# Kernel tuning notes

Measured on AMD Instinct MI355X. Metric: run time of the kernel, lower is better.

Reference implementation:

```python
import jax, jax.numpy as jnp
import numpy as np

# ODEBlock integrates dy/dt = f(t, y) from T0 to T1 with the dopri5 (Dormand-Prince RK45)
# stage structure. torchdiffeq's dopri5 is adaptive; for a jit/vjp-friendly reference we
# run the same 6-stage dopri5 tableau with a fixed number of steps (same per-step math).
T0, T1 = 0.0, 1.0
NUM_STEPS = 16

BATCH, D, H = 512, 1024, 2048


def setup_inputs() -> dict:
    key = jax.random.key(0)
    k0, k1, k2 = jax.random.split(key, 3)
    x = jax.random.normal(k0, (BATCH, D), dtype=jnp.float32)
    W1 = jax.random.normal(k1, (D, H), dtype=jnp.float32) / np.float32(np.sqrt(D))
    b1 = jnp.zeros((H,), dtype=jnp.float32)
    W2 = jax.random.normal(k2, (H, D), dtype=jnp.float32) / np.float32(np.sqrt(H))
    b2 = jnp.zeros((D,), dtype=jnp.float32)
    return {"x": x, "W1": W1, "b1": b1, "W2": W2, "b2": b2}


def reference(x, W1, b1, W2, b2):
    def f(t, y):
        # odefunc: 2-layer tanh MLP, autonomous in t
        return jnp.tanh(y @ W1 + b1) @ W2 + b2

    h = jnp.float32((T1 - T0) / NUM_STEPS)

    def step(carry, _):
        y, t = carry
        k1 = f(t, y)
        k2 = f(t + h * (1.0 / 5.0), y + h * (1.0 / 5.0) * k1)
        k3 = f(t + h * (3.0 / 10.0), y + h * ((3.0 / 40.0) * k1 + (9.0 / 40.0) * k2))
        k4 = f(t + h * (4.0 / 5.0),
               y + h * ((44.0 / 45.0) * k1 - (56.0 / 15.0) * k2 + (32.0 / 9.0) * k3))
        k5 = f(t + h * (8.0 / 9.0),
               y + h * ((19372.0 / 6561.0) * k1 - (25360.0 / 2187.0) * k2
                        + (64448.0 / 6561.0) * k3 - (212.0 / 729.0) * k4))
        k6 = f(t + h,
               y + h * ((9017.0 / 3168.0) * k1 - (355.0 / 33.0) * k2
                        + (46732.0 / 5247.0) * k3 + (49.0 / 176.0) * k4
                        - (5103.0 / 18656.0) * k5))
        # 5th-order solution weights (b7 = 0, so k7/FSAL not needed for the update)
        y_next = y + h * ((35.0 / 384.0) * k1 + (500.0 / 1113.0) * k3
                          + (125.0 / 192.0) * k4 - (2187.0 / 6784.0) * k5
                          + (11.0 / 84.0) * k6)
        return (y_next, t + h), None

    (y_final, _), _ = jax.lax.scan(step, (x, jnp.float32(T0)), None, length=NUM_STEPS)
    return y_final
```

## Files before the change

### kernel.cpp

```cpp
#include <hip/hip_runtime.h>
#include <hip/hip_bf16.h>

using bf16 = __hip_bfloat16;
typedef __attribute__((ext_vector_type(8))) short short8;
typedef __attribute__((ext_vector_type(4))) float f32x4;
typedef __attribute__((ext_vector_type(4))) unsigned short u16x4;

#define MFMA16(A, B, C) __builtin_amdgcn_mfma_f32_16x16x32_bf16(A, B, C, 0, 0, 0)

constexpr int Mdim = 512;
constexpr int Ddim = 1024;
constexpr int Hdim = 2048;
constexpr size_t MH = (size_t)Mdim * Hdim;
constexpr size_t KPLANE = MH / 4;

constexpr double Hs = 1.0 / 16.0;
constexpr float CF[6][6] = {
    {float(Hs * 1 / 5.), 0.f, 0.f, 0.f, 0.f, 0.f},
    {float(Hs * 3 / 40.), float(Hs * 9 / 40.), 0.f, 0.f, 0.f, 0.f},
    {float(Hs * 44 / 45.), float(-Hs * 56 / 15.), float(Hs * 32 / 9.), 0.f, 0.f, 0.f},
    {float(Hs * 19372 / 6561.), float(-Hs * 25360 / 2187.), float(Hs * 64448 / 6561.),
     float(-Hs * 212 / 729.), 0.f, 0.f},
    {float(Hs * 9017 / 3168.), float(-Hs * 355 / 33.), float(Hs * 46732 / 5247.),
     float(Hs * 49 / 176.), float(-Hs * 5103 / 18656.), 0.f},
    {float(Hs * 35 / 384.), 0.f, float(Hs * 500 / 1113.), float(Hs * 125 / 192.),
     float(-Hs * 2187 / 6784.), float(Hs * 11 / 84.)},
};

__device__ __forceinline__ float tanh_fast(float x) {
  float xc = fminf(fmaxf(x, -15.0f), 15.0f);
  float t = __expf(2.0f * xc);
  return (t - 1.0f) * __builtin_amdgcn_rcpf(t + 1.0f);
}

__device__ __forceinline__ unsigned short f2bf(float x) {
  bf16 b = __float2bfloat16(x);
  return *(unsigned short*)&b;
}
__device__ __forceinline__ float bf2f(unsigned short u) {
  bf16 b = *(bf16*)&u;
  return __bfloat162float(b);
}

__device__ __forceinline__ void gload_lds16(const void* g, void* lds) {
  __builtin_amdgcn_global_load_lds((const __attribute__((address_space(1))) void*)g,
                                   (__attribute__((address_space(3))) void*)lds, 16, 0, 0);
}

enum { M_PLAIN = 0, M_INIT = 1, M_STG = 2, M_FINAL = 3 };

struct GArgs {
  const bf16* A;
  const bf16* Bt;
  const float* b1;
  const float* b2w1;
  const float* xin;
  const float* b2;
  float* yW1;
  bf16* T;
  bf16* K;
  float* G;
  bf16* Wout;
  float* y;
};

template <int MODE, int STAGE, int NDIM, int KDIM>
__global__ __launch_bounds__(512, 2) void fused_gemm(GArgs a) {
  constexpr int BK = 128;
  constexpr int NITER = KDIM / BK;
  constexpr int NP = (NDIM / 64) / 8;

  extern __shared__ char smem_c[];

  const int tid = threadIdx.x;
  const int lane = tid & 63;
  const int wid = tid >> 6;
  const int kq = wid & 3;
  const int nh = wid >> 2;
  const int fr = lane & 15;
  const int kg = (lane >> 4) & 3;

  const int bid = blockIdx.x;
  const int nt = (bid & 7) * NP + ((bid >> 3) % NP);
  const int mt = (bid >> 3) / NP;
  const int brow = mt * 64, bcol = nt * 64;
  const int tile = mt * (NDIM / 64) + nt;

  const int rs0 = tid >> 4;
  const int cgS = (tid & 15) ^ (rs0 & 7);
  const bf16* pA0 = a.A + (size_t)(brow + rs0) * KDIM + cgS * 8;
  const bf16* pA1 = pA0 + (size_t)32 * KDIM;
  const bf16* pB0 = a.Bt + (size_t)(bcol + rs0) * KDIM + cgS * 8;
  const bf16* pB1 = pB0 + (size_t)32 * KDIM;
  char* dA = smem_c + tid * 16;
  char* dB = smem_c + 16384 + tid * 16;

#define STAGE_TILE(T_)                                                       \
  {                                                                          \
    const int B_ = ((T_) % 3) * 32768;                                       \
    const int KO_ = (T_)*BK;                                                 \
    gload_lds16(pA0 + KO_, dA + B_); gload_lds16(pA1 + KO_, dA + B_ + 8192); \
    gload_lds16(pB0 + KO_, dB + B_); gload_lds16(pB1 + KO_, dB + B_ + 8192); \
  }

  const int xA = (((kq * 4 + kg) ^ (fr & 7)) << 4);
  const char* rA = smem_c + fr * 256 + xA;
  const char* rB = smem_c + 16384 + (nh * 32 + fr) * 256 + xA;

  f32x4 acc[4][2] = {};

  STAGE_TILE(0)
  STAGE_TILE(1)

#pragma unroll
  for (int t = 0; t < NITER; ++t) {
    if (t < NITER - 1) asm volatile("s_waitcnt vmcnt(4)" ::: "memory");
    else               asm volatile("s_waitcnt vmcnt(0)" ::: "memory");
    __builtin_amdgcn_s_barrier();
    __builtin_amdgcn_sched_barrier(0);
    if (t + 2 < NITER) STAGE_TILE(t + 2)
    const int BO = (t % 3) * 32768;
    short8 af[4], bw[2];
    af[0] = *(const short8*)(rA + BO);
    af[1] = *(const short8*)(rA + BO + 4096);
    af[2] = *(const short8*)(rA + BO + 8192);
    af[3] = *(const short8*)(rA + BO + 12288);
    bw[0] = *(const short8*)(rB + BO);
    bw[1] = *(const short8*)(rB + BO + 4096);
    __builtin_amdgcn_s_setprio(1);
#pragma unroll
    for (int mf = 0; mf < 4; ++mf)
#pragma unroll
      for (int nf = 0; nf < 2; ++nf) acc[mf][nf] = MFMA16(af[mf], bw[nf], acc[mf][nf]);
    __builtin_amdgcn_s_setprio(0);
  }
#undef STAGE_TILE

  __syncthreads();
#pragma unroll
  for (int mf = 0; mf < 4; ++mf)
#pragma unroll
    for (int nf = 0; nf < 2; ++nf)
      *(f32x4*)(smem_c + (((mf * 4 + nh * 2 + nf) * 4 + kq) << 10) + lane * 16) = acc[mf][nf];
  __syncthreads();

#pragma unroll
  for (int of = 0; of < 2; ++of) {
    const int p = wid * 2 + of;
    const int mfo = p >> 2, nfo = p & 3;
    f32x4 s = {};
#pragma unroll
    for (int k = 0; k < 4; ++k)
      s += *(const f32x4*)(smem_c + (((p * 4 + k) << 10)) + lane * 16);

    const int c = bcol + nfo * 16 + fr;
    const int r0 = brow + mfo * 16 + kg * 4;
    if constexpr (MODE == M_PLAIN) {
#pragma unroll
      for (int e = 0; e < 4; ++e) a.Wout[(size_t)(r0 + e) * NDIM + c] = __float2bfloat16(s[e]);
    } else if constexpr (MODE == M_INIT) {
#pragma unroll
      for (int e = 0; e < 4; ++e) {
        const size_t idx = (size_t)(r0 + e) * NDIM + c;
        a.yW1[idx] = s[e];
        const float tv = tanh_fast(s[e] + a.b1[c]);
        a.T[idx] = __float2bfloat16(tv);
        a.G[idx] = CF[5][0] * tv;
      }
    } else if constexpr (MODE == M_STG) {
      u16x4* Kq = (u16x4*)a.K;
      const size_t kbase = (size_t)tile * 1024 + (size_t)p * 64 + lane;
      const float bb = a.b2w1[c];
      float Kv[4], comb[4];
#pragma unroll
      for (int e = 0; e < 4; ++e) Kv[e] = s[e] + bb;
      if constexpr (STAGE <= 5) {
        u16x4 kw;
#pragma unroll
        for (int e = 0; e < 4; ++e) kw[e] = f2bf(Kv[e]);
        Kq[(size_t)(STAGE - 1) * KPLANE + kbase] = kw;
      }
#pragma unroll
      for (int e = 0; e < 4; ++e)
        comb[e] = a.yW1[(size_t)(r0 + e) * NDIM + c] + CF[STAGE - 1][STAGE - 1] * Kv[e];
      if constexpr (STAGE > 1 && CF[STAGE - 1][0] != 0.f) {
        u16x4 kj = Kq[0 * KPLANE + kbase];
#pragma unroll
        for (int e = 0; e < 4; ++e) comb[e] += CF[STAGE - 1][0] * bf2f(kj[e]);
      }
      if constexpr (STAGE > 2 && CF[STAGE - 1][1] != 0.f) {
        u16x4 kj = Kq[1 * KPLANE + kbase];
#pragma unroll
        for (int e = 0; e < 4; ++e) comb[e] += CF[STAGE - 1][1] * bf2f(kj[e]);
      }
      if constexpr (STAGE > 3 && CF[STAGE - 1][2] != 0.f) {
        u16x4 kj = Kq[2 * KPLANE + kbase];
#pragma unroll
        for (int e = 0; e < 4; ++e) comb[e] += CF[STAGE - 1][2] * bf2f(kj[e]);
      }
      if constexpr (STAGE > 4 && CF[STAGE - 1][3] != 0.f) {
        u16x4 kj = Kq[3 * KPLANE + kbase];
#pragma unroll
        for (int e = 0; e < 4; ++e) comb[e] += CF[STAGE - 1][3] * bf2f(kj[e]);
      }
      if constexpr (STAGE > 5 && CF[STAGE - 1][4] != 0.f) {
        u16x4 kj = Kq[4 * KPLANE + kbase];
#pragma unroll
        for (int e = 0; e < 4; ++e) comb[e] += CF[STAGE - 1][4] * bf2f(kj[e]);
      }
#pragma unroll
      for (int e = 0; e < 4; ++e) {
        const size_t idx = (size_t)(r0 + e) * NDIM + c;
        const float tv = tanh_fast(comb[e] + a.b1[c]);
        a.T[idx] = __float2bfloat16(tv);
        if constexpr (STAGE < 6) {
          if constexpr (CF[5][STAGE] != 0.f) a.G[idx] += CF[5][STAGE] * tv;
        } else {
          a.yW1[idx] = comb[e];
          a.G[idx] += CF[5][0] * tv;
        }
      }
    } else {
#pragma unroll
      for (int e = 0; e < 4; ++e) {
        const size_t idx = (size_t)(r0 + e) * NDIM + c;
        a.y[idx] = a.xin[idx] + s[e] + a.b2[c];
      }
    }
  }
}

__global__ void transpose_to_bf16(const float* __restrict__ in, bf16* __restrict__ out, int R,
                                  int C) {
  __shared__ float t[32][33];
  const int c0 = blockIdx.x * 32, r0 = blockIdx.y * 32;
#pragma unroll
  for (int i = threadIdx.y; i < 32; i += 8)
    t[i][threadIdx.x] = in[(size_t)(r0 + i) * C + c0 + threadIdx.x];
  __syncthreads();
#pragma unroll
  for (int i = threadIdx.y; i < 32; i += 8)
    out[(size_t)(c0 + i) * R + r0 + threadIdx.x] = __float2bfloat16(t[threadIdx.x][i]);
}

__global__ void cast_bf16(const float* __restrict__ in, bf16* __restrict__ out, int n4) {
  int i = blockIdx.x * 256 + threadIdx.x;
  if (i < n4) {
    float4 v = *(const float4*)(in + i * 4);
    bf16* o = out + i * 4;
    o[0] = __float2bfloat16(v.x); o[1] = __float2bfloat16(v.y);
    o[2] = __float2bfloat16(v.z); o[3] = __float2bfloat16(v.w);
  }
}

__global__ void b2w1_kernel(const float* __restrict__ b2, const float* __restrict__ W1,
                            float* __restrict__ out) {
  const int h = blockIdx.x * 256 + threadIdx.x;
  float s = 0.f;
  for (int d = 0; d < Ddim; ++d) s += b2[d] * W1[(size_t)d * Hdim + h];
  out[h] = s;
}

extern "C" void kernel_launch(void* const* d_in, const int* in_sizes, int n_in, void* d_out,
                              int out_size, void* d_ws, size_t ws_size, hipStream_t stream) {
  const float* x = (const float*)d_in[0];
  const float* W1 = (const float*)d_in[1];
  const float* b1 = (const float*)d_in[2];
  const float* W2 = (const float*)d_in[3];
  const float* b2 = (const float*)d_in[4];
  float* y = (float*)d_out;

  char* ws = (char*)d_ws;
  bf16* W1t = (bf16*)(ws + 0);
  bf16* W2bf = (bf16*)(ws + (4ull << 20));
  bf16* W2t = (bf16*)(ws + (8ull << 20));
  bf16* W21t = (bf16*)(ws + (12ull << 20));
  bf16* xbf = (bf16*)(ws + (20ull << 20));
  bf16* Tbuf = (bf16*)(ws + (21ull << 20));
  bf16* Kbuf = (bf16*)(ws + (23ull << 20));
  bf16* Gbf = (bf16*)(ws + (33ull << 20));
  float* yW1 = (float*)(ws + (35ull << 20));
  float* Gacc = (float*)(ws + (39ull << 20));
  float* b2w1 = (float*)(ws + (43ull << 20));

  GArgs a = {};
  a.b1 = b1; a.b2w1 = b2w1; a.xin = x; a.b2 = b2;
  a.yW1 = yW1; a.T = Tbuf; a.K = Kbuf; a.G = Gacc; a.y = y;

  constexpr int SMEM = 98304;
  hipFuncSetAttribute((const void*)&fused_gemm<M_PLAIN, 0, Hdim, 1024>,
                      hipFuncAttributeMaxDynamicSharedMemorySize, SMEM);
  hipFuncSetAttribute((const void*)&fused_gemm<M_INIT, 0, Hdim, 1024>,
                      hipFuncAttributeMaxDynamicSharedMemorySize, SMEM);
  hipFuncSetAttribute((const void*)&fused_gemm<M_STG, 1, Hdim, Hdim>,
                      hipFuncAttributeMaxDynamicSharedMemorySize, SMEM);
  hipFuncSetAttribute((const void*)&fused_gemm<M_STG, 2, Hdim, Hdim>,
                      hipFuncAttributeMaxDynamicSharedMemorySize, SMEM);
  hipFuncSetAttribute((const void*)&fused_gemm<M_STG, 3, Hdim, Hdim>,
                      hipFuncAttributeMaxDynamicSharedMemorySize, SMEM);
  hipFuncSetAttribute((const void*)&fused_gemm<M_STG, 4, Hdim, Hdim>,
                      hipFuncAttributeMaxDynamicSharedMemorySize, SMEM);
  hipFuncSetAttribute((const void*)&fused_gemm<M_STG, 5, Hdim, Hdim>,
                      hipFuncAttributeMaxDynamicSharedMemorySize, SMEM);
  hipFuncSetAttribute((const void*)&fused_gemm<M_STG, 6, Hdim, Hdim>,
                      hipFuncAttributeMaxDynamicSharedMemorySize, SMEM);
  hipFuncSetAttribute((const void*)&fused_gemm<M_FINAL, 0, Ddim, Hdim>,
                      hipFuncAttributeMaxDynamicSharedMemorySize, SMEM);

  transpose_to_bf16<<<dim3(Hdim / 32, Ddim / 32), dim3(32, 8), 0, stream>>>(W1, W1t, Ddim, Hdim);
  transpose_to_bf16<<<dim3(Ddim / 32, Hdim / 32), dim3(32, 8), 0, stream>>>(W2, W2t, Hdim, Ddim);
  cast_bf16<<<(Hdim * Ddim / 4 + 255) / 256, 256, 0, stream>>>(W2, W2bf, Hdim * Ddim / 4);
  cast_bf16<<<(Mdim * Ddim / 4 + 255) / 256, 256, 0, stream>>>(x, xbf, Mdim * Ddim / 4);
  b2w1_kernel<<<Hdim / 256, 256, 0, stream>>>(b2, W1, b2w1);

  {
    GArgs p = a; p.A = W1t; p.Bt = W2bf; p.Wout = W21t;
    fused_gemm<M_PLAIN, 0, Hdim, 1024><<<32 * 32, 512, SMEM, stream>>>(p);
  }
  {
    GArgs p = a; p.A = xbf; p.Bt = W1t;
    fused_gemm<M_INIT, 0, Hdim, 1024><<<8 * 32, 512, SMEM, stream>>>(p);
  }

  GArgs sg = a; sg.A = Tbuf; sg.Bt = W21t;
  for (int step = 0; step < 16; ++step) {
    fused_gemm<M_STG, 1, Hdim, Hdim><<<8 * 32, 512, SMEM, stream>>>(sg);
    fused_gemm<M_STG, 2, Hdim, Hdim><<<8 * 32, 512, SMEM, stream>>>(sg);
    fused_gemm<M_STG, 3, Hdim, Hdim><<<8 * 32, 512, SMEM, stream>>>(sg);
    fused_gemm<M_STG, 4, Hdim, Hdim><<<8 * 32, 512, SMEM, stream>>>(sg);
    fused_gemm<M_STG, 5, Hdim, Hdim><<<8 * 32, 512, SMEM, stream>>>(sg);
    if (step < 15)
      fused_gemm<M_STG, 6, Hdim, Hdim><<<8 * 32, 512, SMEM, stream>>>(sg);
  }

  cast_bf16<<<(int)(MH / 4 + 255) / 256, 256, 0, stream>>>(Gacc, Gbf, (int)(MH / 4));
  {
    GArgs p = a; p.A = Gbf; p.Bt = W2t;
    fused_gemm<M_FINAL, 0, Ddim, Hdim><<<8 * 16, 512, SMEM, stream>>>(p);
  }
}
```

Before: 1.380 ms.

## Switch GEMM to 32x32x16 MFMA with 8-way split-K reduction

Replaces the 16x16x32 MFMA tiling (4 k-quarters x 2 n-halves of waves) with 32x32x16 MFMAs where all 8 waves split K and each computes the full 64x64 tile, then reduces 8 partials through LDS. It also switches yW1 to a fragment-ordered vectorized layout so the stage epilogue loads and stores it as f32x4. The aim is fewer LDS fragment reads per MFMA and the higher throughput of the larger MFMA shape. The cost is a larger LDS reduction buffer (SMEM raised to 128KB), which may limit the launch_bounds target of 2 blocks per CU, plus a heavier 8-way reduction.

Result: no change. 1.358 ms (-1.6%).

```diff
diff --git a/kernel.cpp b/kernel.cpp
--- a/kernel.cpp
+++ b/kernel.cpp
@@ -4,15 +4,16 @@
 using bf16 = __hip_bfloat16;
 typedef __attribute__((ext_vector_type(8))) short short8;
 typedef __attribute__((ext_vector_type(4))) float f32x4;
+typedef __attribute__((ext_vector_type(16))) float f32x16;
 typedef __attribute__((ext_vector_type(4))) unsigned short u16x4;
 
-#define MFMA16(A, B, C) __builtin_amdgcn_mfma_f32_16x16x32_bf16(A, B, C, 0, 0, 0)
+#define MFMA32(A, B, C) __builtin_amdgcn_mfma_f32_32x32x16_bf16(A, B, C, 0, 0, 0)
 
 constexpr int Mdim = 512;
 constexpr int Ddim = 1024;
 constexpr int Hdim = 2048;
 constexpr size_t MH = (size_t)Mdim * Hdim;
-constexpr size_t KPLANE = MH / 4;
+constexpr size_t KPL4 = MH / 4;
 
 constexpr double Hs = 1.0 / 16.0;
 constexpr float CF[6][6] = {
@@ -75,10 +76,8 @@
   const int tid = threadIdx.x;
   const int lane = tid & 63;
   const int wid = tid >> 6;
-  const int kq = wid & 3;
-  const int nh = wid >> 2;
-  const int fr = lane & 15;
-  const int kg = (lane >> 4) & 3;
+  const int l31 = lane & 31;
+  const int hi = lane >> 5;
 
   const int bid = blockIdx.x;
   const int nt = (bid & 7) * NP + ((bid >> 3) % NP);
@@ -103,11 +102,11 @@
     gload_lds16(pB0 + KO_, dB + B_); gload_lds16(pB1 + KO_, dB + B_ + 8192); \
   }
 
-  const int xA = (((kq * 4 + kg) ^ (fr & 7)) << 4);
-  const char* rA = smem_c + fr * 256 + xA;
-  const char* rB = smem_c + 16384 + (nh * 32 + fr) * 256 + xA;
-
-  f32x4 acc[4][2] = {};
+  const int xo = l31 * 256 + (((wid * 2 + hi) ^ (l31 & 7)) << 4);
+  const char* rA = smem_c + xo;
+  const char* rB = smem_c + 16384 + xo;
+
+  f32x16 acc[2][2] = {};
 
   STAGE_TILE(0)
   STAGE_TILE(1)
@@ -120,111 +119,120 @@
     __builtin_amdgcn_sched_barrier(0);
     if (t + 2 < NITER) STAGE_TILE(t + 2)
     const int BO = (t % 3) * 32768;
-    short8 af[4], bw[2];
-    af[0] = *(const short8*)(rA + BO);
-    af[1] = *(const short8*)(rA + BO + 4096);
-    af[2] = *(const short8*)(rA + BO + 8192);
-    af[3] = *(const short8*)(rA + BO + 12288);
-    bw[0] = *(const short8*)(rB + BO);
-    bw[1] = *(const short8*)(rB + BO + 4096);
+    short8 af0 = *(const short8*)(rA + BO);
+    short8 af1 = *(const short8*)(rA + BO + 8192);
+    short8 bw0 = *(const short8*)(rB + BO);
+    short8 bw1 = *(const short8*)(rB + BO + 8192);
     __builtin_amdgcn_s_setprio(1);
-#pragma unroll
-    for (int mf = 0; mf < 4; ++mf)
-#pragma unroll
-      for (int nf = 0; nf < 2; ++nf) acc[mf][nf] = MFMA16(af[mf], bw[nf], acc[mf][nf]);
+    acc[0][0] = MFMA32(af0, bw0, acc[0][0]);
+    acc[0][1] = MFMA32(af0, bw1, acc[0][1]);
+    acc[1][0] = MFMA32(af1, bw0, acc[1][0]);
+    acc[1][1] = MFMA32(af1, bw1, acc[1][1]);
     __builtin_amdgcn_s_setprio(0);
   }
 #undef STAGE_TILE
 
   __syncthreads();
 #pragma unroll
-  for (int mf = 0; mf < 4; ++mf)
+  for (int mf = 0; mf < 2; ++mf)
 #pragma unroll
     for (int nf = 0; nf < 2; ++nf)
-      *(f32x4*)(smem_c + (((mf * 4 + nh * 2 + nf) * 4 + kq) << 10) + lane * 16) = acc[mf][nf];
+#pragma unroll
+      for (int g = 0; g < 4; ++g) {
+        f32x4 v = {acc[mf][nf][g * 4 + 0], acc[mf][nf][g * 4 + 1],
+                   acc[mf][nf][g * 4 + 2], acc[mf][nf][g * 4 + 3]};
+        *(f32x4*)(smem_c + ((((mf * 2 + nf) * 4 + g) * 8 + wid) << 10) + lane * 16) = v;
+      }
   __syncthreads();
 
 #pragma unroll
   for (int of = 0; of < 2; ++of) {
-    const int p = wid * 2 + of;
-    const int mfo = p >> 2, nfo = p & 3;
+    const int q = wid * 2 + of;
     f32x4 s = {};
 #pragma unroll
-    for (int k = 0; k < 4; ++k)
-      s += *(const f32x4*)(smem_c + (((p * 4 + k) << 10)) + lane * 16);
-
-    const int c = bcol + nfo * 16 + fr;
-    const int r0 = brow + mfo * 16 + kg * 4;
+    for (int w = 0; w < 8; ++w)
+      s += *(const f32x4*)(smem_c + (((q * 8 + w) << 10)) + lane * 16);
+
+    const int p = q >> 2, g = q & 3;
+    const int mf = p >> 1, nf = p & 1;
+    const int c = bcol + nf * 32 + l31;
+    const int r0 = brow + mf * 32 + g * 8 + hi * 4;
     if constexpr (MODE == M_PLAIN) {
 #pragma unroll
       for (int e = 0; e < 4; ++e) a.Wout[(size_t)(r0 + e) * NDIM + c] = __float2bfloat16(s[e]);
     } else if constexpr (MODE == M_INIT) {
+      ((f32x4*)a.yW1)[(size_t)(tile * 16 + q) * 64 + lane] = s;
+      const float bv = a.b1[c];
 #pragma unroll
       for (int e = 0; e < 4; ++e) {
         const size_t idx = (size_t)(r0 + e) * NDIM + c;
-        a.yW1[idx] = s[e];
-        const float tv = tanh_fast(s[e] + a.b1[c]);
+        const float tv = tanh_fast(s[e] + bv);
         a.T[idx] = __float2bfloat16(tv);
         a.G[idx] = CF[5][0] * tv;
       }
     } else if constexpr (MODE == M_STG) {
       u16x4* Kq = (u16x4*)a.K;
-      const size_t kbase = (size_t)tile * 1024 + (size_t)p * 64 + lane;
+      const size_t kb = (size_t)(tile * 16 + q) * 64 + lane;
       const float bb = a.b2w1[c];
       float Kv[4], comb[4];
+      const f32x4 yv = ((const f32x4*)a.yW1)[kb];
 #pragma unroll
       for (int e = 0; e < 4; ++e) Kv[e] = s[e] + bb;
       if constexpr (STAGE <= 5) {
         u16x4 kw;
 #pragma unroll
         for (int e = 0; e < 4; ++e) kw[e] = f2bf(Kv[e]);
-        Kq[(size_t)(STAGE - 1) * KPLANE + kbase] = kw;
-      }
-#pragma unroll
-      for (int e = 0; e < 4; ++e)
-        comb[e] = a.yW1[(size_t)(r0 + e) * NDIM + c] + CF[STAGE - 1][STAGE - 1] * Kv[e];
+        Kq[(size_t)(STAGE - 1) * KPL4 + kb] = kw;
+      }
+#pragma unroll
+      for (int e = 0; e < 4; ++e) comb[e] = yv[e] + CF[STAGE - 1][STAGE - 1] * Kv[e];
       if constexpr (STAGE > 1 && CF[STAGE - 1][0] != 0.f) {
-        u16x4 kj = Kq[0 * KPLANE + kbase];
+        u16x4 kj = Kq[0 * KPL4 + kb];
 #pragma unroll
         for (int e = 0; e < 4; ++e) comb[e] += CF[STAGE - 1][0] * bf2f(kj[e]);
       }
       if constexpr (STAGE > 2 && CF[STAGE - 1][1] != 0.f) {
-        u16x4 kj = Kq[1 * KPLANE + kbase];
+        u16x4 kj = Kq[1 * KPL4 + kb];
 #pragma unroll
         for (int e = 0; e < 4; ++e) comb[e] += CF[STAGE - 1][1] * bf2f(kj[e]);
       }
       if constexpr (STAGE > 3 && CF[STAGE - 1][2] != 0.f) {
-        u16x4 kj = Kq[2 * KPLANE + kbase];
+        u16x4 kj = Kq[2 * KPL4 + kb];
 #pragma unroll
         for (int e = 0; e < 4; ++e) comb[e] += CF[STAGE - 1][2] * bf2f(kj[e]);
       }
       if constexpr (STAGE > 4 && CF[STAGE - 1][3] != 0.f) {
-        u16x4 kj = Kq[3 * KPLANE + kbase];
+        u16x4 kj = Kq[3 * KPL4 + kb];
 #pragma unroll
         for (int e = 0; e < 4; ++e) comb[e] += CF[STAGE - 1][3] * bf2f(kj[e]);
       }
       if constexpr (STAGE > 5 && CF[STAGE - 1][4] != 0.f) {
-        u16x4 kj = Kq[4 * KPLANE + kbase];
+        u16x4 kj = Kq[4 * KPL4 + kb];
 #pragma unroll
         for (int e = 0; e < 4; ++e) comb[e] += CF[STAGE - 1][4] * bf2f(kj[e]);
       }
+      if constexpr (STAGE == 6) {
+        f32x4 cw = {comb[0], comb[1], comb[2], comb[3]};
+        ((f32x4*)a.yW1)[kb] = cw;
+      }
+      const float bv = a.b1[c];
 #pragma unroll
       for (int e = 0; e < 4; ++e) {
         const size_t idx = (size_t)(r0 + e) * NDIM + c;
-        const float tv = tanh_fast(comb[e] + a.b1[c]);
+        const float tv = tanh_fast(comb[e] + bv);
         a.T[idx] = __float2bfloat16(tv);
         if constexpr (STAGE < 6) {
           if constexpr (CF[5][STAGE] != 0.f) a.G[idx] += CF[5][STAGE] * tv;
         } else {
-          a.yW1[idx] = comb[e];
           a.G[idx] += CF[5][0] * tv;
         }
       }
     } else {
+      const float bv = a.b2[c];
 #pragma unroll
       for (int e = 0; e < 4; ++e) {
         const size_t idx = (size_t)(r0 + e) * NDIM + c;
-        a.y[idx] = a.xin[idx] + s[e] + a.b2[c];
+        a.y[idx] = a.xin[idx] + s[e] + bv;
       }
     }
   }
@@ -287,7 +295,7 @@
   a.b1 = b1; a.b2w1 = b2w1; a.xin = x; a.b2 = b2;
   a.yW1 = yW1; a.T = Tbuf; a.K = Kbuf; a.G = Gacc; a.y = y;
 
-  constexpr int SMEM = 98304;
+  constexpr int SMEM = 131072;
   hipFuncSetAttribute((const void*)&fused_gemm<M_PLAIN, 0, Hdim, 1024>,
                       hipFuncAttributeMaxDynamicSharedMemorySize, SMEM);
   hipFuncSetAttribute((const void*)&fused_gemm<M_INIT, 0, Hdim, 1024>,
```
